# Kernel tuning notes

Measured on AMD Instinct MI355X. Metric: run time of the kernel, lower is better.

## Reference

```python
import jax, jax.numpy as jnp
import numpy as np

IN_BIT = 8
W_BIT = 8
B, CIN, COUT = 4096, 2048, 2048


def _uq(x, k):
    # uniform_quantize forward math (k-bit fake quantization)
    n = float(2 ** k - 1)
    return jnp.round(x * n) / n


def setup_inputs() -> dict:
    key = jax.random.key(0)
    k1, k2 = jax.random.split(key)
    x = jax.random.uniform(k1, (B, CIN), dtype=jnp.float32)  # inputs in [0,1] (clamped by quantizer)
    # kaiming-normal-like init for weight [COUT, CIN]
    weight = jax.random.normal(k2, (COUT, CIN), dtype=jnp.float32) * np.float32((2.0 / CIN) ** 0.5)
    # default (unassigned) phases: first half -pi/2, second half +pi/2
    half = CIN // 2
    phases = jnp.concatenate(
        [jnp.full((1, 1, half), -np.pi / 2, dtype=jnp.float32),
         jnp.full((1, 1, CIN - half), np.pi / 2, dtype=jnp.float32)], axis=2)
    disks = jnp.ones((1, 1, CIN, 2), dtype=jnp.float32)
    return {"x": x, "weight": weight, "phases": phases, "disks": disks}


def reference(x, weight, phases, disks):
    # --- input quantization: uniform_q(clamp(x,0,1)) ---
    xq = _uq(jnp.clip(x, 0.0, 1.0), IN_BIT)                      # [B, CIN]
    # --- weight quantization (dorefa): tanh, normalize to [0,1], quantize ---
    w = jnp.tanh(weight)
    w = w / (2.0 * jnp.max(jnp.abs(w))) + 0.5
    wq = _uq(w, W_BIT)                                            # [COUT, CIN]
    # --- optical (homodyne) linear with phase/disk modulation ---
    # out = 0.25 * sum_i (I+ - I-)
    # With ideal phases (sin = +/-1) and unit disks this reduces to x @ (w * sign).T
    sin_phi = jnp.sin(phases)[0, 0]                               # [CIN]
    d0 = disks[0, 0, :, 0]
    d1 = disks[0, 0, :, 1]
    dd = d0 - d1                                                  # [CIN]
    ds = d0 + d1                                                  # [CIN]
    term_x = (xq * xq) @ dd                                       # [B]
    term_w = (wq * wq) @ dd                                       # [COUT]
    cross = jnp.einsum('bi,oi->bo', xq, wq * (sin_phi * ds))      # [B, COUT]
    out = 0.25 * (term_x[:, None] + term_w[None, :] + 2.0 * cross)
    return out
```

## Files before the change

### kernel.cpp

```cpp
#include <hip/hip_runtime.h>
#include <hip/hip_bf16.h>
#include <math.h>

#define B_DIM 4096
#define CIN   2048
#define COUT  2048

typedef float f32x4  __attribute__((ext_vector_type(4)));
typedef int   i32x4  __attribute__((ext_vector_type(4)));
typedef int   i32x16 __attribute__((ext_vector_type(16)));
typedef char  c8x8   __attribute__((ext_vector_type(8)));

__device__ inline float wave_reduce_sum(float v) {
#pragma unroll
    for (int off = 32; off > 0; off >>= 1)
        v += __shfl_down(v, off, 64);
    return v;
}
__device__ inline float wave_reduce_max(float v) {
#pragma unroll
    for (int off = 32; off > 0; off >>= 1)
        v = fmaxf(v, __shfl_down(v, off, 64));
    return v;
}

#define NMAXBLK 256
__global__ void prep_k1_kernel(const float* __restrict__ weight,
                               const float* __restrict__ phases,
                               const float* __restrict__ disks,
                               float* __restrict__ pmax,
                               float* __restrict__ s_tab,
                               float* __restrict__ dd_tab,
                               float* __restrict__ smax_buf) {
    __shared__ float red[4];
    const int blk = blockIdx.x;
    const int tid = threadIdx.x;

    if (blk < NMAXBLK) {
        const size_t n4 = (size_t)COUT * CIN / 4;
        const f32x4* w4 = (const f32x4*)weight;
        float m = 0.f;
        for (size_t i = (size_t)blk * 256 + tid; i < n4; i += (size_t)NMAXBLK * 256) {
            f32x4 v = w4[i];
            m = fmaxf(m, fmaxf(fmaxf(fabsf(v[0]), fabsf(v[1])),
                               fmaxf(fabsf(v[2]), fabsf(v[3]))));
        }
        m = wave_reduce_max(m);
        if ((tid & 63) == 0) red[tid >> 6] = m;
        __syncthreads();
        if (tid == 0)
            pmax[blk] = fmaxf(fmaxf(red[0], red[1]), fmaxf(red[2], red[3]));
    } else {
        float lmax = 0.f;
        for (int i = tid; i < CIN; i += 256) {
            float d0 = disks[2 * i], d1 = disks[2 * i + 1];
            float s  = sinf(phases[i]) * (d0 + d1);
            s_tab[i]  = s;
            dd_tab[i] = d0 - d1;
            lmax = fmaxf(lmax, fabsf(s));
        }
        lmax = wave_reduce_max(lmax);
        if ((tid & 63) == 0) red[tid >> 6] = lmax;
        __syncthreads();
        if (tid == 0)
            smax_buf[0] = fmaxf(fmaxf(fmaxf(red[0], red[1]),
                                      fmaxf(red[2], red[3])), 1e-20f);
    }
}

__global__ void prep_k2_kernel(const float* __restrict__ x,
                               const float* __restrict__ weight,
                               const float* __restrict__ disks,
                               const float* __restrict__ pmax,
                               const float* __restrict__ s_tab,
                               const float* __restrict__ dd_tab,
                               const float* __restrict__ smax_buf,
                               char* __restrict__ XQ8,
                               float* __restrict__ term_x,
                               char* __restrict__ V8,
                               float* __restrict__ term_w2) {
    __shared__ float red[4];
    const int blk = blockIdx.x;
    const int tid = threadIdx.x;

    if (blk < B_DIM) {
        const float* xr = x + (size_t)blk * CIN + tid * 8;
        const f32x4* dk = (const f32x4*)(disks + (size_t)tid * 16);
        f32x4 v0 = ((const f32x4*)xr)[0];
        f32x4 v1 = ((const f32x4*)xr)[1];
        c8x8 h;
        float sum = 0.f;
#pragma unroll
        for (int j = 0; j < 8; ++j) {
            float xv = (j < 4) ? v0[j] : v1[j - 4];
            float qr = rintf(fminf(fmaxf(xv, 0.f), 1.f) * 255.f);
            float q  = qr * (1.f / 255.f);
            f32x4 dv = dk[j >> 1];
            float d0 = dv[(j & 1) * 2], d1 = dv[(j & 1) * 2 + 1];
            sum += q * q * (d0 - d1);
            h[j] = (char)(int)(qr - 128.f);
        }
        *(c8x8*)(XQ8 + (size_t)blk * CIN + tid * 8) = h;
        sum = wave_reduce_sum(sum);
        if ((tid & 63) == 0) red[tid >> 6] = sum;
        __syncthreads();
        if (tid == 0)
            term_x[blk] = 0.25f * (red[0] + red[1] + red[2] + red[3]);
    } else {
        __shared__ float bmax;
        float m = pmax[tid];
        m = wave_reduce_max(m);
        if ((tid & 63) == 0) red[tid >> 6] = m;
        __syncthreads();
        if (tid == 0)
            bmax = tanhf(fmaxf(fmaxf(red[0], red[1]), fmaxf(red[2], red[3])));
        __syncthreads();
        const float inv2m = 0.5f / bmax;
        const float smax  = smax_buf[0];
        const float k127  = 127.f / smax;

        const int o = blk - B_DIM;
        const f32x4* w4  = (const f32x4*)(weight + (size_t)o * CIN + tid * 8);
        const f32x4* s4  = (const f32x4*)(s_tab  + tid * 8);
        const f32x4* dd4 = (const f32x4*)(dd_tab + tid * 8);
        float sumdd = 0.f, sb = 0.f;
        c8x8 h;
#pragma unroll
        for (int half = 0; half < 2; ++half) {
            f32x4 wv = w4[half], sv = s4[half], ddv = dd4[half];
#pragma unroll
            for (int j = 0; j < 4; ++j) {
                float t  = tanhf(wv[j]);
                float wq = rintf((t * inv2m + 0.5f) * 255.f) * (1.f / 255.f);
                sumdd += wq * wq * ddv[j];
                float bp = rintf(wq * sv[j] * k127);
                sb += bp;
                h[half * 4 + j] = (char)(int)bp;
            }
        }
        *(c8x8*)(V8 + (size_t)o * CIN + tid * 8) = h;

        sumdd = wave_reduce_sum(sumdd);
        sb    = wave_reduce_sum(sb);
        __syncthreads();
        if ((tid & 63) == 0) red[tid >> 6] = sumdd;
        __syncthreads();
        float sumdd_t = red[0] + red[1] + red[2] + red[3];
        __syncthreads();
        if ((tid & 63) == 0) red[tid >> 6] = sb;
        __syncthreads();
        if (tid == 0) {
            float sb_t = red[0] + red[1] + red[2] + red[3];
            term_w2[o] = 0.25f * sumdd_t + (64.f * smax / 32385.f) * sb_t;
        }
    }
}

#define BM 128
#define BN 128
#define BKB 64
#define NT (CIN / BKB)

#define MEMFENCE asm volatile("" ::: "memory")
#define BARRIER() do { MEMFENCE; __builtin_amdgcn_s_barrier(); MEMFENCE; } while (0)
#define VMCNT(N) asm volatile("s_waitcnt vmcnt(" #N ")" ::: "memory")

__global__ __launch_bounds__(256, 2) void
gemm_kernel(const char* __restrict__ A,
            const char* __restrict__ Bw,
            const float* __restrict__ term_x,
            const float* __restrict__ term_w2,
            const float* __restrict__ smax_buf,
            float* __restrict__ C) {
    __shared__ __align__(16) char As[3][BM * BKB];
    __shared__ __align__(16) char Bs[3][BN * BKB];

    const int tid  = threadIdx.x;
    const int wave = tid >> 6;
    const int lane = tid & 63;

    const int wg  = blockIdx.x;
    const int xcd = wg & 7;
    const int idx = wg >> 3;
    const int tile_m = (xcd >> 1) * 8 + (idx >> 3);
    const int tile_n = (xcd & 1) * 8 + (idx & 7);
    const int row0 = tile_m * BM;
    const int col0 = tile_n * BN;
    const int wr = wave >> 1;
    const int wc = wave & 1;

    i32x16 acc[2][2];
#pragma unroll
    for (int m = 0; m < 2; ++m)
#pragma unroll
        for (int n = 0; n < 2; ++n)
#pragma unroll
            for (int j = 0; j < 16; ++j)
                acc[m][n][j] = 0;

    const int st_row = lane >> 2;
    const int st_sc  = ((lane & 3) ^ ((lane >> 3) & 3)) * 16;
    const char* Agp = A  + (size_t)row0 * CIN;
    const char* Bgp = Bw + (size_t)col0 * CIN;

    const int rl = lane & 31;
    const int hi = lane >> 5;
    const int fx = (rl >> 1) & 3;

    int offA[2][2], offB[2][2];
#pragma unroll
    for (int ks = 0; ks < 2; ++ks)
#pragma unroll
        for (int m = 0; m < 2; ++m) {
            const int pg = ((ks * 2 + hi) ^ fx) * 16;
            offA[ks][m] = (wr * 64 + m * 32 + rl) * BKB + pg;
            offB[ks][m] = (wc * 64 + m * 32 + rl) * BKB + pg;
        }

#define STAGE(buf, k0) do {                                                    \
    _Pragma("unroll")                                                          \
    for (int j = 0; j < 2; ++j) {           \
        const int chunk = wave + j * 4;                                        \
        const int rr = chunk * 16 + st_row;                                    \
        __builtin_amdgcn_global_load_lds(                                      \
            (const __attribute__((address_space(1))) void*)(Agp + (size_t)rr * CIN + (k0) + st_sc), \
            (__attribute__((address_space(3))) void*)(&As[buf][chunk * 1024]), \
            16, 0, 0);                                                         \
        __builtin_amdgcn_global_load_lds(                                      \
            (const __attribute__((address_space(1))) void*)(Bgp + (size_t)rr * CIN + (k0) + st_sc), \
            (__attribute__((address_space(3))) void*)(&Bs[buf][chunk * 1024]), \
            16, 0, 0);                                                         \
    } } while (0)

#define TILE(bufc, STAGE_STMT, VM_STMT) do {                                   \
    STAGE_STMT;                                                                \
    _Pragma("unroll")                                                          \
    for (int ks = 0; ks < 2; ++ks) {                                           \
        i32x4 a0 = *(const i32x4*)(&As[bufc][offA[ks][0]]);                    \
        i32x4 a1 = *(const i32x4*)(&As[bufc][offA[ks][1]]);                    \
        i32x4 b0 = *(const i32x4*)(&Bs[bufc][offB[ks][0]]);                    \
        i32x4 b1 = *(const i32x4*)(&Bs[bufc][offB[ks][1]]);                    \
        __builtin_amdgcn_s_setprio(1);                                         \
        acc[0][0] = __builtin_amdgcn_mfma_i32_32x32x32_i8(a0, b0, acc[0][0], 0, 0, 0); \
        acc[0][1] = __builtin_amdgcn_mfma_i32_32x32x32_i8(a0, b1, acc[0][1], 0, 0, 0); \
        acc[1][0] = __builtin_amdgcn_mfma_i32_32x32x32_i8(a1, b0, acc[1][0], 0, 0, 0); \
        acc[1][1] = __builtin_amdgcn_mfma_i32_32x32x32_i8(a1, b1, acc[1][1], 0, 0, 0); \
        __builtin_amdgcn_s_setprio(0);                                         \
    }                                                                          \
    VM_STMT;                                                                   \
    BARRIER();                                                                 \
} while (0)

    STAGE(0, 0);
    STAGE(1, BKB);
    VMCNT(4);
    BARRIER();

    int k0 = 0;
#pragma unroll 1
    for (int grp = 0; grp < 10; ++grp) {
        TILE(0, STAGE(2, k0 + 2 * BKB), VMCNT(4));
        TILE(1, STAGE(0, k0 + 3 * BKB), VMCNT(4));
        TILE(2, STAGE(1, k0 + 4 * BKB), VMCNT(4));
        k0 += 3 * BKB;
    }
    TILE(0, (void)0, VMCNT(0));
    TILE(1, (void)0, (void)0);

    const float coef = 0.5f * smax_buf[0] / 32385.f;
#pragma unroll
    for (int m = 0; m < 2; ++m)
#pragma unroll
        for (int n = 0; n < 2; ++n) {
            const int c = col0 + wc * 64 + n * 32 + rl;
            const float tw = term_w2[c];
#pragma unroll
            for (int reg = 0; reg < 16; ++reg) {
                const int r = row0 + wr * 64 + m * 32 +
                              (reg & 3) + 8 * (reg >> 2) + 4 * hi;
                C[(size_t)r * COUT + c] =
                    coef * (float)acc[m][n][reg] + term_x[r] + tw;
            }
        }
#undef STAGE
#undef TILE
}

extern "C" void kernel_launch(void* const* d_in, const int* in_sizes, int n_in,
                              void* d_out, int out_size, void* d_ws, size_t ws_size,
                              hipStream_t stream) {
    const float* x      = (const float*)d_in[0];
    const float* weight = (const float*)d_in[1];
    const float* phases = (const float*)d_in[2];
    const float* disks  = (const float*)d_in[3];
    float* out = (float*)d_out;

    char* ws = (char*)d_ws;
    float* pmax     = (float*)(ws);
    float* smax_buf = (float*)(ws + 1024);
    float* s_tab    = (float*)(ws + 4096);
    float* dd_tab   = (float*)(ws + 16384);
    float* term_w2  = (float*)(ws + 32768);
    float* term_x   = (float*)(ws + 49152);
    char* XQ8 = (char*)(ws + 65536);
    char* V8  = (char*)(ws + 65536 + (size_t)B_DIM * CIN);

    prep_k1_kernel<<<NMAXBLK + 1, 256, 0, stream>>>(
        weight, phases, disks, pmax, s_tab, dd_tab, smax_buf);
    prep_k2_kernel<<<B_DIM + COUT, 256, 0, stream>>>(
        x, weight, disks, pmax, s_tab, dd_tab, smax_buf,
        XQ8, term_x, V8, term_w2);
    gemm_kernel<<<(B_DIM / BM) * (COUT / BN), 256, 0, stream>>>(
        XQ8, V8, term_x, term_w2, smax_buf, out);
}
```

Baseline: 50.06 us.

## Use eight waves per GEMM block with 64x32 per-wave output tiles

Doubles the GEMM workgroup from 256 to 512 threads, arranging the waves 2x4 so each computes a 64x32 sub-tile with two accumulators instead of a 64x64 tile with four. Each wave now issues a single staging load per operand per k-step, and the waitcnt thresholds are adjusted to match. The intent is more waves in flight to hide LDS and global latency and to lower per-wave register pressure. The cost is more barrier participants and less B-fragment reuse per wave, so each wave does more LDS reads per MFMA.

```diff
diff --git a/kernel.cpp b/kernel.cpp
--- a/kernel.cpp
+++ b/kernel.cpp
@@ -165,7 +165,7 @@
 #define BARRIER() do { MEMFENCE; __builtin_amdgcn_s_barrier(); MEMFENCE; } while (0)
 #define VMCNT(N) asm volatile("s_waitcnt vmcnt(" #N ")" ::: "memory")
 
-__global__ __launch_bounds__(256, 2) void
+__global__ __launch_bounds__(512, 2) void
 gemm_kernel(const char* __restrict__ A,
             const char* __restrict__ Bw,
             const float* __restrict__ term_x,
@@ -186,17 +186,12 @@
     const int tile_n = (xcd & 1) * 8 + (idx & 7);
     const int row0 = tile_m * BM;
     const int col0 = tile_n * BN;
-    const int wr = wave >> 1;
-    const int wc = wave & 1;
-
-    i32x16 acc[2][2];
-#pragma unroll
-    for (int m = 0; m < 2; ++m)
-#pragma unroll
-        for (int n = 0; n < 2; ++n)
-#pragma unroll
-            for (int j = 0; j < 16; ++j)
-                acc[m][n][j] = 0;
+    const int wr = wave >> 2;
+    const int wc = wave & 3;
+
+    i32x16 acc0, acc1;
+#pragma unroll
+    for (int j = 0; j < 16; ++j) { acc0[j] = 0; acc1[j] = 0; }
 
     const int st_row = lane >> 2;
     const int st_sc  = ((lane & 3) ^ ((lane >> 3) & 3)) * 16;
@@ -207,30 +202,27 @@
     const int hi = lane >> 5;
     const int fx = (rl >> 1) & 3;
 
-    int offA[2][2], offB[2][2];
-#pragma unroll
-    for (int ks = 0; ks < 2; ++ks)
-#pragma unroll
-        for (int m = 0; m < 2; ++m) {
-            const int pg = ((ks * 2 + hi) ^ fx) * 16;
+    int offA[2][2], offB[2];
+#pragma unroll
+    for (int ks = 0; ks < 2; ++ks) {
+        const int pg = ((ks * 2 + hi) ^ fx) * 16;
+#pragma unroll
+        for (int m = 0; m < 2; ++m)
             offA[ks][m] = (wr * 64 + m * 32 + rl) * BKB + pg;
-            offB[ks][m] = (wc * 64 + m * 32 + rl) * BKB + pg;
-        }
+        offB[ks] = (wc * 32 + rl) * BKB + pg;
+    }
 
 #define STAGE(buf, k0) do {                                                    \
-    _Pragma("unroll")                                                          \
-    for (int j = 0; j < 2; ++j) {           \
-        const int chunk = wave + j * 4;                                        \
-        const int rr = chunk * 16 + st_row;                                    \
-        __builtin_amdgcn_global_load_lds(                                      \
-            (const __attribute__((address_space(1))) void*)(Agp + (size_t)rr * CIN + (k0) + st_sc), \
-            (__attribute__((address_space(3))) void*)(&As[buf][chunk * 1024]), \
-            16, 0, 0);                                                         \
-        __builtin_amdgcn_global_load_lds(                                      \
-            (const __attribute__((address_space(1))) void*)(Bgp + (size_t)rr * CIN + (k0) + st_sc), \
-            (__attribute__((address_space(3))) void*)(&Bs[buf][chunk * 1024]), \
-            16, 0, 0);                                                         \
-    } } while (0)
+    const int rr = wave * 16 + st_row;          \
+    __builtin_amdgcn_global_load_lds(                                          \
+        (const __attribute__((address_space(1))) void*)(Agp + (size_t)rr * CIN + (k0) + st_sc), \
+        (__attribute__((address_space(3))) void*)(&As[buf][wave * 1024]),      \
+        16, 0, 0);                                                             \
+    __builtin_amdgcn_global_load_lds(                                          \
+        (const __attribute__((address_space(1))) void*)(Bgp + (size_t)rr * CIN + (k0) + st_sc), \
+        (__attribute__((address_space(3))) void*)(&Bs[buf][wave * 1024]),      \
+        16, 0, 0);                                                             \
+} while (0)
 
 #define TILE(bufc, STAGE_STMT, VM_STMT) do {                                   \
     STAGE_STMT;                                                                \
@@ -238,13 +230,10 @@
     for (int ks = 0; ks < 2; ++ks) {                                           \
         i32x4 a0 = *(const i32x4*)(&As[bufc][offA[ks][0]]);                    \
         i32x4 a1 = *(const i32x4*)(&As[bufc][offA[ks][1]]);                    \
-        i32x4 b0 = *(const i32x4*)(&Bs[bufc][offB[ks][0]]);                    \
-        i32x4 b1 = *(const i32x4*)(&Bs[bufc][offB[ks][1]]);                    \
+        i32x4 b0 = *(const i32x4*)(&Bs[bufc][offB[ks]]);                       \
         __builtin_amdgcn_s_setprio(1);                                         \
-        acc[0][0] = __builtin_amdgcn_mfma_i32_32x32x32_i8(a0, b0, acc[0][0], 0, 0, 0); \
-        acc[0][1] = __builtin_amdgcn_mfma_i32_32x32x32_i8(a0, b1, acc[0][1], 0, 0, 0); \
-        acc[1][0] = __builtin_amdgcn_mfma_i32_32x32x32_i8(a1, b0, acc[1][0], 0, 0, 0); \
-        acc[1][1] = __builtin_amdgcn_mfma_i32_32x32x32_i8(a1, b1, acc[1][1], 0, 0, 0); \
+        acc0 = __builtin_amdgcn_mfma_i32_32x32x32_i8(a0, b0, acc0, 0, 0, 0);   \
+        acc1 = __builtin_amdgcn_mfma_i32_32x32x32_i8(a1, b0, acc1, 0, 0, 0);   \
         __builtin_amdgcn_s_setprio(0);                                         \
     }                                                                          \
     VM_STMT;                                                                   \
@@ -253,35 +242,34 @@
 
     STAGE(0, 0);
     STAGE(1, BKB);
-    VMCNT(4);
+    VMCNT(2);
     BARRIER();
 
     int k0 = 0;
 #pragma unroll 1
     for (int grp = 0; grp < 10; ++grp) {
-        TILE(0, STAGE(2, k0 + 2 * BKB), VMCNT(4));
-        TILE(1, STAGE(0, k0 + 3 * BKB), VMCNT(4));
-        TILE(2, STAGE(1, k0 + 4 * BKB), VMCNT(4));
+        TILE(0, STAGE(2, k0 + 2 * BKB), VMCNT(2));
+        TILE(1, STAGE(0, k0 + 3 * BKB), VMCNT(2));
+        TILE(2, STAGE(1, k0 + 4 * BKB), VMCNT(2));
         k0 += 3 * BKB;
     }
     TILE(0, (void)0, VMCNT(0));
     TILE(1, (void)0, (void)0);
 
     const float coef = 0.5f * smax_buf[0] / 32385.f;
-#pragma unroll
-    for (int m = 0; m < 2; ++m)
-#pragma unroll
-        for (int n = 0; n < 2; ++n) {
-            const int c = col0 + wc * 64 + n * 32 + rl;
-            const float tw = term_w2[c];
-#pragma unroll
-            for (int reg = 0; reg < 16; ++reg) {
-                const int r = row0 + wr * 64 + m * 32 +
-                              (reg & 3) + 8 * (reg >> 2) + 4 * hi;
-                C[(size_t)r * COUT + c] =
-                    coef * (float)acc[m][n][reg] + term_x[r] + tw;
-            }
-        }
+    const int c = col0 + wc * 32 + rl;
+    const float tw = term_w2[c];
+#pragma unroll
+    for (int m = 0; m < 2; ++m) {
+        const i32x16* am = (m == 0) ? &acc0 : &acc1;
+#pragma unroll
+        for (int reg = 0; reg < 16; ++reg) {
+            const int r = row0 + wr * 64 + m * 32 +
+                          (reg & 3) + 8 * (reg >> 2) + 4 * hi;
+            C[(size_t)r * COUT + c] =
+                coef * (float)((*am)[reg]) + term_x[r] + tw;
+        }
+    }
 #undef STAGE
 #undef TILE
 }
@@ -310,6 +298,6 @@
     prep_k2_kernel<<<B_DIM + COUT, 256, 0, stream>>>(
         x, weight, disks, pmax, s_tab, dd_tab, smax_buf,
         XQ8, term_x, V8, term_w2);
-    gemm_kernel<<<(B_DIM / BM) * (COUT / BN), 256, 0, stream>>>(
+    gemm_kernel<<<(B_DIM / BM) * (COUT / BN), 512, 0, stream>>>(
         XQ8, V8, term_x, term_w2, smax_buf, out);
 }
```

Result: no change. 49.90 us (-0.3%).

## Replace LDS triple-buffered pipeline with direct global-to-register MFMA operand loads

Applied to the files above, without the earlier changes.

Removes the shared-memory staging (global_load_lds triple buffering, barriers, vmcnt waits) and has each wave load its i8 MFMA operands straight from global memory into registers, with the K loop fully unrolled. It is meant to remove LDS traffic and barrier synchronisation overhead. In exchange, waves that share rows no longer share tiles, so global/L2 traffic per block roughly doubles. Loads are also only partially coalesced (16-byte pieces per row), and the full unroll over 16 iterations raises register pressure.

```diff
diff --git a/kernel.cpp b/kernel.cpp
--- a/kernel.cpp
+++ b/kernel.cpp
@@ -158,23 +158,15 @@
 
 #define BM 128
 #define BN 128
-#define BKB 64
-#define NT (CIN / BKB)
-
-#define MEMFENCE asm volatile("" ::: "memory")
-#define BARRIER() do { MEMFENCE; __builtin_amdgcn_s_barrier(); MEMFENCE; } while (0)
-#define VMCNT(N) asm volatile("s_waitcnt vmcnt(" #N ")" ::: "memory")
-
-__global__ __launch_bounds__(256, 2) void
+#define NT (CIN / 128)
+
+__global__ __launch_bounds__(256) void
 gemm_kernel(const char* __restrict__ A,
             const char* __restrict__ Bw,
             const float* __restrict__ term_x,
             const float* __restrict__ term_w2,
             const float* __restrict__ smax_buf,
             float* __restrict__ C) {
-    __shared__ __align__(16) char As[3][BM * BKB];
-    __shared__ __align__(16) char Bs[3][BN * BKB];
-
     const int tid  = threadIdx.x;
     const int wave = tid >> 6;
     const int lane = tid & 63;
@@ -189,6 +181,14 @@
     const int wr = wave >> 1;
     const int wc = wave & 1;
 
+    const int rl = lane & 31;
+    const int hi = lane >> 5;
+
+    const char* Ab0 = A  + (size_t)(row0 + wr * 64 +      rl) * CIN + hi * 16;
+    const char* Ab1 = A  + (size_t)(row0 + wr * 64 + 32 + rl) * CIN + hi * 16;
+    const char* Bb0 = Bw + (size_t)(col0 + wc * 64 +      rl) * CIN + hi * 16;
+    const char* Bb1 = Bw + (size_t)(col0 + wc * 64 + 32 + rl) * CIN + hi * 16;
+
     i32x16 acc[2][2];
 #pragma unroll
     for (int m = 0; m < 2; ++m)
@@ -198,74 +198,21 @@
             for (int j = 0; j < 16; ++j)
                 acc[m][n][j] = 0;
 
-    const int st_row = lane >> 2;
-    const int st_sc  = ((lane & 3) ^ ((lane >> 3) & 3)) * 16;
-    const char* Agp = A  + (size_t)row0 * CIN;
-    const char* Bgp = Bw + (size_t)col0 * CIN;
-
-    const int rl = lane & 31;
-    const int hi = lane >> 5;
-    const int fx = (rl >> 1) & 3;
-
-    int offA[2][2], offB[2][2];
-#pragma unroll
-    for (int ks = 0; ks < 2; ++ks)
-#pragma unroll
-        for (int m = 0; m < 2; ++m) {
-            const int pg = ((ks * 2 + hi) ^ fx) * 16;
-            offA[ks][m] = (wr * 64 + m * 32 + rl) * BKB + pg;
-            offB[ks][m] = (wc * 64 + m * 32 + rl) * BKB + pg;
-        }
-
-#define STAGE(buf, k0) do {                                                    \
-    _Pragma("unroll")                                                          \
-    for (int j = 0; j < 2; ++j) {           \
-        const int chunk = wave + j * 4;                                        \
-        const int rr = chunk * 16 + st_row;                                    \
-        __builtin_amdgcn_global_load_lds(                                      \
-            (const __attribute__((address_space(1))) void*)(Agp + (size_t)rr * CIN + (k0) + st_sc), \
-            (__attribute__((address_space(3))) void*)(&As[buf][chunk * 1024]), \
-            16, 0, 0);                                                         \
-        __builtin_amdgcn_global_load_lds(                                      \
-            (const __attribute__((address_space(1))) void*)(Bgp + (size_t)rr * CIN + (k0) + st_sc), \
-            (__attribute__((address_space(3))) void*)(&Bs[buf][chunk * 1024]), \
-            16, 0, 0);                                                         \
-    } } while (0)
-
-#define TILE(bufc, STAGE_STMT, VM_STMT) do {                                   \
-    STAGE_STMT;                                                                \
-    _Pragma("unroll")                                                          \
-    for (int ks = 0; ks < 2; ++ks) {                                           \
-        i32x4 a0 = *(const i32x4*)(&As[bufc][offA[ks][0]]);                    \
-        i32x4 a1 = *(const i32x4*)(&As[bufc][offA[ks][1]]);                    \
-        i32x4 b0 = *(const i32x4*)(&Bs[bufc][offB[ks][0]]);                    \
-        i32x4 b1 = *(const i32x4*)(&Bs[bufc][offB[ks][1]]);                    \
-        __builtin_amdgcn_s_setprio(1);                                         \
-        acc[0][0] = __builtin_amdgcn_mfma_i32_32x32x32_i8(a0, b0, acc[0][0], 0, 0, 0); \
-        acc[0][1] = __builtin_amdgcn_mfma_i32_32x32x32_i8(a0, b1, acc[0][1], 0, 0, 0); \
-        acc[1][0] = __builtin_amdgcn_mfma_i32_32x32x32_i8(a1, b0, acc[1][0], 0, 0, 0); \
-        acc[1][1] = __builtin_amdgcn_mfma_i32_32x32x32_i8(a1, b1, acc[1][1], 0, 0, 0); \
-        __builtin_amdgcn_s_setprio(0);                                         \
-    }                                                                          \
-    VM_STMT;                                                                   \
-    BARRIER();                                                                 \
-} while (0)
-
-    STAGE(0, 0);
-    STAGE(1, BKB);
-    VMCNT(4);
-    BARRIER();
-
-    int k0 = 0;
-#pragma unroll 1
-    for (int grp = 0; grp < 10; ++grp) {
-        TILE(0, STAGE(2, k0 + 2 * BKB), VMCNT(4));
-        TILE(1, STAGE(0, k0 + 3 * BKB), VMCNT(4));
-        TILE(2, STAGE(1, k0 + 4 * BKB), VMCNT(4));
-        k0 += 3 * BKB;
+#pragma unroll
+    for (int t = 0; t < NT; ++t) {
+#pragma unroll
+        for (int ks = 0; ks < 4; ++ks) {
+            const int off = t * 128 + ks * 32;
+            i32x4 a0 = *(const i32x4*)(Ab0 + off);
+            i32x4 a1 = *(const i32x4*)(Ab1 + off);
+            i32x4 b0 = *(const i32x4*)(Bb0 + off);
+            i32x4 b1 = *(const i32x4*)(Bb1 + off);
+            acc[0][0] = __builtin_amdgcn_mfma_i32_32x32x32_i8(a0, b0, acc[0][0], 0, 0, 0);
+            acc[0][1] = __builtin_amdgcn_mfma_i32_32x32x32_i8(a0, b1, acc[0][1], 0, 0, 0);
+            acc[1][0] = __builtin_amdgcn_mfma_i32_32x32x32_i8(a1, b0, acc[1][0], 0, 0, 0);
+            acc[1][1] = __builtin_amdgcn_mfma_i32_32x32x32_i8(a1, b1, acc[1][1], 0, 0, 0);
+        }
     }
-    TILE(0, (void)0, VMCNT(0));
-    TILE(1, (void)0, (void)0);
 
     const float coef = 0.5f * smax_buf[0] / 32385.f;
 #pragma unroll
@@ -282,8 +229,6 @@
                     coef * (float)acc[m][n][reg] + term_x[r] + tw;
             }
         }
-#undef STAGE
-#undef TILE
 }
 
 extern "C" void kernel_launch(void* const* d_in, const int* in_sizes, int n_in,
```

Measured after the change: 87.44 us. +74.7%, slower.
